# Performance work log

Hardware: AMD Instinct MI355X
Metric: run time of the kernel (lower is better)

## Reference

```python
import jax, jax.numpy as jnp
import numpy as np

H, N, SEQ = 256, 64, 4096

def setup_inputs() -> dict:
    key = jax.random.key(0)
    kA, kB, kC, kdt = jax.random.split(key, 4)
    W = jax.random.normal(kA, (H, N, N), dtype=jnp.float32)
    # Hurwitz (stable) A: skew-symmetric part minus 0.5*I, like HiPPO-style stable transitions
    A = 0.5 * (W - jnp.swapaxes(W, -1, -2)) - 0.5 * jnp.eye(N, dtype=jnp.float32)
    B = jax.random.normal(kB, (H, N), dtype=jnp.float32)
    C = jax.random.normal(kC, (H, N), dtype=jnp.float32)
    # log_dt around log(0.01), matching typical S4 timescale init
    log_dt = jax.random.normal(kdt, (H,), dtype=jnp.float32) * 0.5 + jnp.log(0.01)
    return {"A": A, "B": B, "C": C, "log_dt": log_dt, "L": SEQ}

def _bilinear(dt, A, B):
    # dt: (H,), A: (H,N,N), B: (H,N)
    n = A.shape[-1]
    I = jnp.eye(n, dtype=A.dtype)
    A_back = I - (dt[:, None, None] / 2) * A   # (H,N,N)
    A_fwd = I + (dt[:, None, None] / 2) * A    # (H,N,N)
    dA = jnp.linalg.solve(A_back, A_fwd)                       # (H,N,N)
    dB = dt[:, None] * jnp.linalg.solve(A_back, B[..., None])[..., 0]  # (H,N)
    return dA, dB

def _krylov(L, dA, dB, C):
    # K[h, l] = C[h] @ dA[h]^l @ dB[h], computed by squaring/doubling
    x = dB[..., None]  # (H, N, 1)
    A_ = dA
    while x.shape[-1] < L:
        x2 = jnp.einsum('hmn,hnl->hml', A_, x)  # apply current power
        x = jnp.concatenate([x, x2], axis=-1)
        if x.shape[-1] < L:
            A_ = jnp.einsum('hmn,hnk->hmk', A_, A_)  # square the power
    x = x[..., :L]  # (H, N, L)
    return jnp.einsum('hn,hnl->hl', C, x)  # (H, L)

def reference(A, B, C, log_dt, L):
    dt = jnp.exp(log_dt)
    dA, dB = _bilinear(dt, A, B)
    return _krylov(L, dA, dB, C)
```

## Files before the change

kernel.cpp:

```cpp
#include <hip/hip_runtime.h>

constexpr int STRU = 68;

typedef short v8s __attribute__((ext_vector_type(8)));
typedef float v4f __attribute__((ext_vector_type(4)));

__device__ __forceinline__ int swz(int i, int j) {
    return i * STRU + (j ^ ((i & 8) << 1));
}

__device__ __forceinline__ unsigned packhl(float x) {
    unsigned xb = __builtin_bit_cast(unsigned, x);
    unsigned hb = xb & 0xffff0000u;
    float lof = x - __builtin_bit_cast(float, hb);
    unsigned lb = __builtin_bit_cast(unsigned, lof) + 0x8000u;
    return __builtin_amdgcn_perm(xb, lb, 0x07060302u);
}

__device__ __forceinline__ float unpackf(unsigned v) {
    float h = __builtin_bit_cast(float, v & 0xffff0000u);
    float l = __builtin_bit_cast(float, v << 16);
    return h + l;
}

__device__ __forceinline__ void load_frag(const unsigned* p, v8s& hi, v8s& lo) {
    uint4 a = *(const uint4*)p;
    uint4 b = *(const uint4*)(p + 4);
    uint4 hw, lw;
    hw.x = __builtin_amdgcn_perm(a.y, a.x, 0x07060302u);
    hw.y = __builtin_amdgcn_perm(a.w, a.z, 0x07060302u);
    hw.z = __builtin_amdgcn_perm(b.y, b.x, 0x07060302u);
    hw.w = __builtin_amdgcn_perm(b.w, b.z, 0x07060302u);
    lw.x = __builtin_amdgcn_perm(a.y, a.x, 0x05040100u);
    lw.y = __builtin_amdgcn_perm(a.w, a.z, 0x05040100u);
    lw.z = __builtin_amdgcn_perm(b.y, b.x, 0x05040100u);
    lw.w = __builtin_amdgcn_perm(b.w, b.z, 0x05040100u);
    hi = __builtin_bit_cast(v8s, hw);
    lo = __builtin_bit_cast(v8s, lw);
}

__device__ __forceinline__ void load_col_frag(const unsigned* Q, int col, int kbase,
                                              v8s& hi, v8s& lo) {
    unsigned x[8];
    #pragma unroll
    for (int j = 0; j < 8; ++j) x[j] = Q[swz(kbase + j, col)];
    uint4 hw, lw;
    hw.x = __builtin_amdgcn_perm(x[1], x[0], 0x07060302u);
    hw.y = __builtin_amdgcn_perm(x[3], x[2], 0x07060302u);
    hw.z = __builtin_amdgcn_perm(x[5], x[4], 0x07060302u);
    hw.w = __builtin_amdgcn_perm(x[7], x[6], 0x07060302u);
    lw.x = __builtin_amdgcn_perm(x[1], x[0], 0x05040100u);
    lw.y = __builtin_amdgcn_perm(x[3], x[2], 0x05040100u);
    lw.z = __builtin_amdgcn_perm(x[5], x[4], 0x05040100u);
    lw.w = __builtin_amdgcn_perm(x[7], x[6], 0x05040100u);
    hi = __builtin_bit_cast(v8s, hw);
    lo = __builtin_bit_cast(v8s, lw);
}

#define MFMA16 __builtin_amdgcn_mfma_f32_16x16x32_bf16

template<bool BCOL>
__device__ __forceinline__ v4f tile16(const unsigned* __restrict__ P,
                                      const unsigned* __restrict__ Q,
                                      int rb, int cb, int lane) {
    const int nh = lane & 15, qd = lane >> 4;
    v4f a0 = {0, 0, 0, 0}, a1 = {0, 0, 0, 0};
    #pragma unroll
    for (int kk = 0; kk < 2; ++kk) {
        const int kc = kk * 32 + qd * 8;
        v8s ph, pl, qh, ql;
        load_frag(P + swz(rb + nh, kc), ph, pl);
        if constexpr (BCOL) load_col_frag(Q, cb + nh, kc, qh, ql);
        else                load_frag(Q + swz(cb + nh, kc), qh, ql);
        a0 = MFMA16(ph, qh, a0, 0, 0, 0);
        a1 = MFMA16(ph, ql, a1, 0, 0, 0);
        a1 = MFMA16(pl, qh, a1, 0, 0, 0);
    }
    return a0 + a1;
}

__launch_bounds__(1024)
__global__ void krylov_kernel(const float* __restrict__ A,
                              const float* __restrict__ Bv,
                              const float* __restrict__ Cv,
                              const float* __restrict__ logdt,
                              float* __restrict__ out)
{
    const int h    = blockIdx.x;
    const int tid  = threadIdx.x;
    const int lane = tid & 63;
    const int w    = tid >> 6;
    const int nh   = lane & 15, qd = lane >> 4;
    const int rb   = (w >> 2) * 16, cb = (w & 3) * 16;

    __shared__ __align__(16) unsigned W0[64 * STRU], W1[64 * STRU],
                                      W2[64 * STRU], W3[64 * STRU];
    __shared__ float Bl[64], Cl[64], tmv[64];

    const float dt  = expf(logdt[h]);
    const float c   = 0.5f * dt;
    const float al  = 1.0f + 0.5f * c;
    const float sd2 = (c * c) / (al * al);
    const float c1  = 2.0f / al;
    const float c2  = 2.0f * c / (al * al);
    const float k1  = dt / al;
    const float k2  = dt * c / (al * al);

    const float* Ah = A + (size_t)h * 4096;

    {
        const int rr = tid >> 4, c0 = (tid & 15) * 4;
        float4 v = *(const float4*)(Ah + rr * 64 + c0);
        if (rr == c0 + 0) v.x += 0.5f;
        if (rr == c0 + 1) v.y += 0.5f;
        if (rr == c0 + 2) v.z += 0.5f;
        if (rr == c0 + 3) v.w += 0.5f;
        uint4 pk = make_uint4(packhl(v.x), packhl(v.y), packhl(v.z), packhl(v.w));
        *(uint4*)&W0[swz(rr, c0)] = pk;
        if (tid < 64) Bl[tid] = Bv[h * 64 + tid];
        else if (tid < 128) Cl[tid - 64] = Cv[h * 64 + (tid - 64)];
    }
    __syncthreads();

    {
        v4f a = tile16<true>(W0, W0, rb, cb, lane);
        #pragma unroll
        for (int e = 0; e < 4; ++e) {
            const int row = rb + qd * 4 + e, col = cb + nh;
            float dv = sd2 * a[e];
            W1[swz(row, col)] = packhl(dv);
            W2[swz(row, col)] = packhl(dv + (row == col ? 1.0f : 0.0f));
        }
    }
    __syncthreads();
    {
        v4f a = tile16<true>(W1, W2, rb, cb, lane);
        #pragma unroll
        for (int e = 0; e < 4; ++e) {
            const int row = rb + qd * 4 + e, col = cb + nh;
            W3[swz(row, col)] = packhl(a[e] + (row == col ? 1.0f : 0.0f));
        }
    }
    __syncthreads();
    {
        v4f a = tile16<true>(W1, W3, rb, cb, lane);
        #pragma unroll
        for (int e = 0; e < 4; ++e) {
            const int row = rb + qd * 4 + e, col = cb + nh;
            W2[swz(row, col)] = packhl(a[e] + (row == col ? 1.0f : 0.0f));
        }
    }
    __syncthreads();
    {
        v4f a = tile16<true>(W1, W2, rb, cb, lane);
        #pragma unroll
        for (int e = 0; e < 4; ++e) {
            const int row = rb + qd * 4 + e, col = cb + nh;
            W3[swz(row, col)] = packhl(a[e] + (row == col ? 1.0f : 0.0f));
        }
    }
    __syncthreads();
    {
        v4f a = tile16<true>(W0, W3, rb, cb, lane);
        #pragma unroll
        for (int e = 0; e < 4; ++e) {
            const int row = rb + qd * 4 + e, col = cb + nh;
            float t = unpackf(W3[swz(row, col)]);
            W1[swz(row, col)] = packhl(c1 * t - (row == col ? 1.0f : 0.0f)
                                       + c2 * a[e]);
        }
        if (w == 0) {
            float acc1 = 0.0f;
            #pragma unroll
            for (int m4 = 0; m4 < 16; ++m4) {
                uint4 tv = *(const uint4*)&W3[swz(lane, 4 * m4)];
                float4 b4 = *(const float4*)&Bl[4 * m4];
                acc1 += unpackf(tv.x) * b4.x + unpackf(tv.y) * b4.y
                      + unpackf(tv.z) * b4.z + unpackf(tv.w) * b4.w;
            }
            tmv[lane] = acc1;
            __threadfence_block();
            float acc2 = 0.0f;
            #pragma unroll
            for (int m4 = 0; m4 < 16; ++m4) {
                uint4 sv = *(const uint4*)&W0[swz(lane, 4 * m4)];
                float4 t4 = *(const float4*)&tmv[4 * m4];
                acc2 += unpackf(sv.x) * t4.x + unpackf(sv.y) * t4.y
                      + unpackf(sv.z) * t4.z + unpackf(sv.w) * t4.w;
            }
            W2[swz(0, lane)] = packhl(k1 * acc1 + k2 * acc2);
        }
    }
    __syncthreads();

    unsigned* cur = W1;
    unsigned* nxt = W0;
    #pragma unroll 1
    for (int s = 0; s < 12; ++s) {
        if (s < 11) {
            v4f a = tile16<true>(cur, cur, rb, cb, lane);
            #pragma unroll
            for (int e = 0; e < 4; ++e)
                nxt[swz(rb + qd * 4 + e, cb + nh)] = packhl(a[e]);
        }
        const int p2 = (s < 6) ? s : s - 6;
        const int k  = 1 << p2;
        const int ndb = (k > 16) ? 8 : 4;
        if (w < ndb) {
            const int rt = (w >> 2) * 16, tc = (w & 3) * 16;
            unsigned* Xt = (s < 6) ? W2 : W3;
            v4f a = (s < 6) ? tile16<false>(Xt, cur, rt, tc, lane)
                            : tile16<true >(Xt, cur, rt, tc, lane);
            #pragma unroll
            for (int e = 0; e < 4; ++e) {
                const int j = rt + qd * 4 + e;
                if (j < k) Xt[swz(k + j, tc + nh)] = packhl(a[e]);
            }
        }
        if (s == 0 && w == 15) W3[swz(0, lane)] = packhl(Cl[lane]);
        __syncthreads();
        if (s < 11) { unsigned* t = cur; cur = nxt; nxt = t; }
    }

    {
        v4f a = tile16<false>(W3, W2, rb, cb, lane);
        float* oh = out + (size_t)h * 4096;
        #pragma unroll
        for (int e = 0; e < 4; ++e)
            oh[(rb + qd * 4 + e) * 64 + cb + nh] = a[e];
    }
}

extern "C" void kernel_launch(void* const* d_in, const int* in_sizes, int n_in,
                              void* d_out, int out_size, void* d_ws, size_t ws_size,
                              hipStream_t stream) {
    const float* A  = (const float*)d_in[0];
    const float* B  = (const float*)d_in[1];
    const float* C  = (const float*)d_in[2];
    const float* ld = (const float*)d_in[3];
    float* out = (float*)d_out;
    const int H = in_sizes[3];
    krylov_kernel<<<H, 1024, 0, stream>>>(A, B, C, ld, out);
}
```

Before: 82.40 us.

## Halve block size, keep transposed copies to avoid column gathers, split squaring and Krylov waves

```diff
diff --git a/kernel.cpp b/kernel.cpp
--- a/kernel.cpp
+++ b/kernel.cpp
@@ -4,10 +4,6 @@
 
 typedef short v8s __attribute__((ext_vector_type(8)));
 typedef float v4f __attribute__((ext_vector_type(4)));
-
-__device__ __forceinline__ int swz(int i, int j) {
-    return i * STRU + (j ^ ((i & 8) << 1));
-}
 
 __device__ __forceinline__ unsigned packhl(float x) {
     unsigned xb = __builtin_bit_cast(unsigned, x);
@@ -39,47 +35,37 @@
     lo = __builtin_bit_cast(v8s, lw);
 }
 
-__device__ __forceinline__ void load_col_frag(const unsigned* Q, int col, int kbase,
-                                              v8s& hi, v8s& lo) {
-    unsigned x[8];
+#define MFMA16 __builtin_amdgcn_mfma_f32_16x16x32_bf16
+
+template<int NT>
+__device__ __forceinline__ void strip_acc(const unsigned* __restrict__ P,
+                                          const unsigned* __restrict__ Q,
+                                          int rb, int t0, int lane, v4f* acc) {
+    const int nh = lane & 15, qd = lane >> 4;
+    v8s ah[2], al[2];
+    load_frag(P + (rb + nh) * STRU + qd * 8,      ah[0], al[0]);
+    load_frag(P + (rb + nh) * STRU + 32 + qd * 8, ah[1], al[1]);
+    v8s bh[NT][2], bl[NT][2];
     #pragma unroll
-    for (int j = 0; j < 8; ++j) x[j] = Q[swz(kbase + j, col)];
-    uint4 hw, lw;
-    hw.x = __builtin_amdgcn_perm(x[1], x[0], 0x07060302u);
-    hw.y = __builtin_amdgcn_perm(x[3], x[2], 0x07060302u);
-    hw.z = __builtin_amdgcn_perm(x[5], x[4], 0x07060302u);
-    hw.w = __builtin_amdgcn_perm(x[7], x[6], 0x07060302u);
-    lw.x = __builtin_amdgcn_perm(x[1], x[0], 0x05040100u);
-    lw.y = __builtin_amdgcn_perm(x[3], x[2], 0x05040100u);
-    lw.z = __builtin_amdgcn_perm(x[5], x[4], 0x05040100u);
-    lw.w = __builtin_amdgcn_perm(x[7], x[6], 0x05040100u);
-    hi = __builtin_bit_cast(v8s, hw);
-    lo = __builtin_bit_cast(v8s, lw);
-}
-
-#define MFMA16 __builtin_amdgcn_mfma_f32_16x16x32_bf16
-
-template<bool BCOL>
-__device__ __forceinline__ v4f tile16(const unsigned* __restrict__ P,
-                                      const unsigned* __restrict__ Q,
-                                      int rb, int cb, int lane) {
-    const int nh = lane & 15, qd = lane >> 4;
-    v4f a0 = {0, 0, 0, 0}, a1 = {0, 0, 0, 0};
+    for (int t = 0; t < NT; ++t) {
+        const unsigned* qr = Q + ((t0 + t) * 16 + nh) * STRU;
+        load_frag(qr + qd * 8,      bh[t][0], bl[t][0]);
+        load_frag(qr + 32 + qd * 8, bh[t][1], bl[t][1]);
+    }
     #pragma unroll
-    for (int kk = 0; kk < 2; ++kk) {
-        const int kc = kk * 32 + qd * 8;
-        v8s ph, pl, qh, ql;
-        load_frag(P + swz(rb + nh, kc), ph, pl);
-        if constexpr (BCOL) load_col_frag(Q, cb + nh, kc, qh, ql);
-        else                load_frag(Q + swz(cb + nh, kc), qh, ql);
-        a0 = MFMA16(ph, qh, a0, 0, 0, 0);
-        a1 = MFMA16(ph, ql, a1, 0, 0, 0);
-        a1 = MFMA16(pl, qh, a1, 0, 0, 0);
-    }
-    return a0 + a1;
-}
-
-__launch_bounds__(1024)
+    for (int t = 0; t < NT; ++t) {
+        v4f a0 = {0, 0, 0, 0}, a1 = {0, 0, 0, 0};
+        #pragma unroll
+        for (int kk = 0; kk < 2; ++kk) {
+            a0 = MFMA16(ah[kk], bh[t][kk], a0, 0, 0, 0);
+            a1 = MFMA16(ah[kk], bl[t][kk], a1, 0, 0, 0);
+            a1 = MFMA16(al[kk], bh[t][kk], a1, 0, 0, 0);
+        }
+        acc[t] = a0 + a1;
+    }
+}
+
+__launch_bounds__(512)
 __global__ void krylov_kernel(const float* __restrict__ A,
                               const float* __restrict__ Bv,
                               const float* __restrict__ Cv,
@@ -91,10 +77,9 @@
     const int lane = tid & 63;
     const int w    = tid >> 6;
     const int nh   = lane & 15, qd = lane >> 4;
-    const int rb   = (w >> 2) * 16, cb = (w & 3) * 16;
-
-    __shared__ __align__(16) unsigned W0[64 * STRU], W1[64 * STRU],
-                                      W2[64 * STRU], W3[64 * STRU];
+
+    __shared__ __align__(16) unsigned B0[64 * STRU], B1[64 * STRU], B2[64 * STRU],
+                                      B3[64 * STRU], B4[64 * STRU], B5[64 * STRU];
     __shared__ float Bl[64], Cl[64], tmv[64];
 
     const float dt  = expf(logdt[h]);
@@ -108,126 +93,153 @@
 
     const float* Ah = A + (size_t)h * 4096;
 
-    {
-        const int rr = tid >> 4, c0 = (tid & 15) * 4;
+    for (int idx = tid; idx < 1024; idx += 512) {
+        const int rr = idx >> 4, c0 = (idx & 15) * 4;
         float4 v = *(const float4*)(Ah + rr * 64 + c0);
         if (rr == c0 + 0) v.x += 0.5f;
         if (rr == c0 + 1) v.y += 0.5f;
         if (rr == c0 + 2) v.z += 0.5f;
         if (rr == c0 + 3) v.w += 0.5f;
         uint4 pk = make_uint4(packhl(v.x), packhl(v.y), packhl(v.z), packhl(v.w));
-        *(uint4*)&W0[swz(rr, c0)] = pk;
-        if (tid < 64) Bl[tid] = Bv[h * 64 + tid];
-        else if (tid < 128) Cl[tid - 64] = Cv[h * 64 + (tid - 64)];
-    }
-    __syncthreads();
-
-    {
-        v4f a = tile16<true>(W0, W0, rb, cb, lane);
-        #pragma unroll
-        for (int e = 0; e < 4; ++e) {
-            const int row = rb + qd * 4 + e, col = cb + nh;
-            float dv = sd2 * a[e];
-            W1[swz(row, col)] = packhl(dv);
-            W2[swz(row, col)] = packhl(dv + (row == col ? 1.0f : 0.0f));
-        }
-    }
-    __syncthreads();
-    {
-        v4f a = tile16<true>(W1, W2, rb, cb, lane);
-        #pragma unroll
-        for (int e = 0; e < 4; ++e) {
-            const int row = rb + qd * 4 + e, col = cb + nh;
-            W3[swz(row, col)] = packhl(a[e] + (row == col ? 1.0f : 0.0f));
-        }
-    }
-    __syncthreads();
-    {
-        v4f a = tile16<true>(W1, W3, rb, cb, lane);
-        #pragma unroll
-        for (int e = 0; e < 4; ++e) {
-            const int row = rb + qd * 4 + e, col = cb + nh;
-            W2[swz(row, col)] = packhl(a[e] + (row == col ? 1.0f : 0.0f));
-        }
-    }
-    __syncthreads();
-    {
-        v4f a = tile16<true>(W1, W2, rb, cb, lane);
-        #pragma unroll
-        for (int e = 0; e < 4; ++e) {
-            const int row = rb + qd * 4 + e, col = cb + nh;
-            W3[swz(row, col)] = packhl(a[e] + (row == col ? 1.0f : 0.0f));
-        }
-    }
-    __syncthreads();
-    {
-        v4f a = tile16<true>(W0, W3, rb, cb, lane);
-        #pragma unroll
-        for (int e = 0; e < 4; ++e) {
-            const int row = rb + qd * 4 + e, col = cb + nh;
-            float t = unpackf(W3[swz(row, col)]);
-            W1[swz(row, col)] = packhl(c1 * t - (row == col ? 1.0f : 0.0f)
-                                       + c2 * a[e]);
-        }
-        if (w == 0) {
-            float acc1 = 0.0f;
-            #pragma unroll
-            for (int m4 = 0; m4 < 16; ++m4) {
-                uint4 tv = *(const uint4*)&W3[swz(lane, 4 * m4)];
-                float4 b4 = *(const float4*)&Bl[4 * m4];
-                acc1 += unpackf(tv.x) * b4.x + unpackf(tv.y) * b4.y
-                      + unpackf(tv.z) * b4.z + unpackf(tv.w) * b4.w;
-            }
-            tmv[lane] = acc1;
-            __threadfence_block();
-            float acc2 = 0.0f;
-            #pragma unroll
-            for (int m4 = 0; m4 < 16; ++m4) {
-                uint4 sv = *(const uint4*)&W0[swz(lane, 4 * m4)];
-                float4 t4 = *(const float4*)&tmv[4 * m4];
-                acc2 += unpackf(sv.x) * t4.x + unpackf(sv.y) * t4.y
-                      + unpackf(sv.z) * t4.z + unpackf(sv.w) * t4.w;
-            }
-            W2[swz(0, lane)] = packhl(k1 * acc1 + k2 * acc2);
-        }
-    }
-    __syncthreads();
-
-    unsigned* cur = W1;
-    unsigned* nxt = W0;
+        *(uint4*)&B1[rr * STRU + c0] = pk;
+    }
+    if (tid < 64) Bl[tid] = Bv[h * 64 + tid];
+    else if (tid < 128) Cl[tid - 64] = Cv[h * 64 + (tid - 64)];
+    __syncthreads();
+
+    const int hrb = 16 * (w & 3), ht0 = 2 * (w >> 2);
+
+    {
+        v4f a[2]; strip_acc<2>(B1, B1, hrb, ht0, lane, a);
+        #pragma unroll
+        for (int t = 0; t < 2; ++t)
+            #pragma unroll
+            for (int e = 0; e < 4; ++e) {
+                const int row = hrb + 4 * qd + e, col = (ht0 + t) * 16 + nh;
+                float dv = -sd2 * a[t][e];
+                B3[row * STRU + col] = packhl(dv);
+                B4[row * STRU + col] = packhl(dv + (row == col ? 1.0f : 0.0f));
+            }
+    }
+    __syncthreads();
+    {
+        v4f a[2]; strip_acc<2>(B3, B4, hrb, ht0, lane, a);
+        #pragma unroll
+        for (int t = 0; t < 2; ++t)
+            #pragma unroll
+            for (int e = 0; e < 4; ++e) {
+                const int row = hrb + 4 * qd + e, col = (ht0 + t) * 16 + nh;
+                B5[row * STRU + col] = packhl(a[t][e] + (row == col ? 1.0f : 0.0f));
+            }
+    }
+    __syncthreads();
+    {
+        v4f a[2]; strip_acc<2>(B3, B5, hrb, ht0, lane, a);
+        #pragma unroll
+        for (int t = 0; t < 2; ++t)
+            #pragma unroll
+            for (int e = 0; e < 4; ++e) {
+                const int row = hrb + 4 * qd + e, col = (ht0 + t) * 16 + nh;
+                B4[row * STRU + col] = packhl(a[t][e] + (row == col ? 1.0f : 0.0f));
+            }
+    }
+    __syncthreads();
+    {
+        v4f a[2]; strip_acc<2>(B3, B4, hrb, ht0, lane, a);
+        #pragma unroll
+        for (int t = 0; t < 2; ++t)
+            #pragma unroll
+            for (int e = 0; e < 4; ++e) {
+                const int row = hrb + 4 * qd + e, col = (ht0 + t) * 16 + nh;
+                B5[row * STRU + col] = packhl(a[t][e] + (row == col ? 1.0f : 0.0f));
+            }
+    }
+    __syncthreads();
+    if (w < 4) {
+        v4f a[4]; strip_acc<4>(B1, B5, 16 * w, 0, lane, a);
+        #pragma unroll
+        for (int t = 0; t < 4; ++t)
+            #pragma unroll
+            for (int e = 0; e < 4; ++e) {
+                const int row = 16 * w + 4 * qd + e, col = t * 16 + nh;
+                float tv = unpackf(B5[row * STRU + col]);
+                float base = c1 * tv - (row == col ? 1.0f : 0.0f);
+                float sv   = c2 * a[t][e];
+                B0[row * STRU + col] = packhl(base + sv);
+                B2[row * STRU + col] = packhl(base - sv);
+            }
+    } else if (w == 4) {
+        float acc1 = 0.0f;
+        #pragma unroll
+        for (int m4 = 0; m4 < 16; ++m4) {
+            uint4 tv = *(const uint4*)&B5[lane * STRU + 4 * m4];
+            float4 b4 = *(const float4*)&Bl[4 * m4];
+            acc1 += unpackf(tv.x) * b4.x + unpackf(tv.y) * b4.y
+                  + unpackf(tv.z) * b4.z + unpackf(tv.w) * b4.w;
+        }
+        tmv[lane] = acc1;
+        __threadfence_block();
+        float acc2 = 0.0f;
+        #pragma unroll
+        for (int m4 = 0; m4 < 16; ++m4) {
+            uint4 sv = *(const uint4*)&B1[lane * STRU + 4 * m4];
+            float4 t4 = *(const float4*)&tmv[4 * m4];
+            acc2 += unpackf(sv.x) * t4.x + unpackf(sv.y) * t4.y
+                  + unpackf(sv.z) * t4.z + unpackf(sv.w) * t4.w;
+        }
+        B4[lane] = packhl(k1 * acc1 + k2 * acc2);
+    }
+    __syncthreads();
+
+    unsigned *bX = B0, *bXT = B2, *bN = B1, *bNT = B3;
     #pragma unroll 1
-    for (int s = 0; s < 12; ++s) {
-        if (s < 11) {
-            v4f a = tile16<true>(cur, cur, rb, cb, lane);
+    for (int p = 0; p < 12; ++p) {
+        if (w < 4) {
+            if (p < 11) {
+                v4f a[4]; strip_acc<4>(bX, bXT, 16 * w, 0, lane, a);
+                #pragma unroll
+                for (int t = 0; t < 4; ++t) {
+                    uint4 tp;
+                    #pragma unroll
+                    for (int e = 0; e < 4; ++e) {
+                        unsigned pk = packhl(a[t][e]);
+                        bN[(16 * w + 4 * qd + e) * STRU + t * 16 + nh] = pk;
+                        ((unsigned*)&tp)[e] = pk;
+                    }
+                    *(uint4*)&bNT[(t * 16 + nh) * STRU + 16 * w + 4 * qd] = tp;
+                }
+            }
+        } else {
+            const bool isV = (p < 6);
+            const int  k   = 1 << (isV ? p : p - 6);
+            unsigned*  Kt  = isV ? B4 : B5;
+            const unsigned* M = isV ? bX : bXT;
+            const int ntr = (k + 15) >> 4;
+            for (int tr = 0; tr < ntr; ++tr) {
+                v4f a[1]; strip_acc<1>(Kt, M, tr * 16, w - 4, lane, a);
+                #pragma unroll
+                for (int e = 0; e < 4; ++e) {
+                    const int j = tr * 16 + 4 * qd + e;
+                    if (j < k) Kt[(k + j) * STRU + (w - 4) * 16 + nh] = packhl(a[0][e]);
+                }
+            }
+            if (p == 0 && w == 4) B5[lane] = packhl(Cl[lane]);
+        }
+        __syncthreads();
+        if (p < 11) {
+            unsigned* t0_ = bX;  bX  = bN;  bN  = t0_;
+            t0_ = bXT; bXT = bNT; bNT = t0_;
+        }
+    }
+
+    {
+        v4f a[2]; strip_acc<2>(B5, B4, hrb, ht0, lane, a);
+        float* oh = out + (size_t)h * 4096;
+        #pragma unroll
+        for (int t = 0; t < 2; ++t)
             #pragma unroll
             for (int e = 0; e < 4; ++e)
-                nxt[swz(rb + qd * 4 + e, cb + nh)] = packhl(a[e]);
-        }
-        const int p2 = (s < 6) ? s : s - 6;
-        const int k  = 1 << p2;
-        const int ndb = (k > 16) ? 8 : 4;
-        if (w < ndb) {
-            const int rt = (w >> 2) * 16, tc = (w & 3) * 16;
-            unsigned* Xt = (s < 6) ? W2 : W3;
-            v4f a = (s < 6) ? tile16<false>(Xt, cur, rt, tc, lane)
-                            : tile16<true >(Xt, cur, rt, tc, lane);
-            #pragma unroll
-            for (int e = 0; e < 4; ++e) {
-                const int j = rt + qd * 4 + e;
-                if (j < k) Xt[swz(k + j, tc + nh)] = packhl(a[e]);
-            }
-        }
-        if (s == 0 && w == 15) W3[swz(0, lane)] = packhl(Cl[lane]);
-        __syncthreads();
-        if (s < 11) { unsigned* t = cur; cur = nxt; nxt = t; }
-    }
-
-    {
-        v4f a = tile16<false>(W3, W2, rb, cb, lane);
-        float* oh = out + (size_t)h * 4096;
-        #pragma unroll
-        for (int e = 0; e < 4; ++e)
-            oh[(rb + qd * 4 + e) * 64 + cb + nh] = a[e];
+                oh[(hrb + 4 * qd + e) * 64 + (ht0 + t) * 16 + nh] = a[t][e];
     }
 }
 
@@ -240,5 +252,5 @@
     const float* ld = (const float*)d_in[3];
     float* out = (float*)d_out;
     const int H = in_sizes[3];
-    krylov_kernel<<<H, 1024, 0, stream>>>(A, B, C, ld, out);
-}
+    krylov_kernel<<<H, 512, 0, stream>>>(A, B, C, ld, out);
+}
```

Measured after the change: 79.71 us. -3.3%, faster.
